# Performance work log

Hardware: AMD Instinct MI355X
Metric: run time of the kernel (lower is better)

The kernel has to match this reference:

```python
import jax, jax.numpy as jnp
import numpy as np

DIM = 256      # C
TOPK = 32      # topk_win_num
WIN = 8        # winSize
G = 64         # g (shift group size); 4*G == DIM here


def setup_inputs() -> dict:
    key = jax.random.key(0)
    k0, k1, k2, k3 = jax.random.split(key, 4)
    B, Nt, Ns, C = 32, 256, 4096, DIM
    z = jax.random.normal(k0, (B, Nt, C), jnp.float32)
    x = jax.random.normal(k1, (B, Ns, C), jnp.float32)
    # shift_op_down: Conv2d(C, 4g, 1) -> weight [4g, C]; shift_op_up: Conv2d(4g, C, 1)
    Wd = jax.random.normal(k2, (4 * G, C), jnp.float32) * 0.05
    bd = jnp.zeros((4 * G,), jnp.float32)
    Wu = jax.random.normal(k3, (C, 4 * G), jnp.float32) * 0.05
    bu = jnp.zeros((C,), jnp.float32)
    return {"z": z, "x": x, "Wd": Wd, "bd": bd, "Wu": Wu, "bu": bu}


def reference(z, x, Wd, bd, Wu, bu):
    B, Nt, C = z.shape
    Ns = x.shape[1]
    hs = int(np.sqrt(Ns))
    wn = hs // WIN          # windows per side
    wsa = WIN * WIN         # tokens per window
    K = TOPK

    # AdaptiveMaxPool2d((1,1)) over template tokens -> global max per channel
    z_max = jnp.max(z, axis=1)                               # [B, C]
    sim = jnp.einsum('bc,bnc->bn', z_max, x) / C             # [B, Ns]
    # per-window mean similarity
    sim = sim.reshape(B, wn, WIN, wn, WIN).transpose(0, 1, 3, 2, 4)
    sim = sim.reshape(B, wn * wn, wsa).mean(-1)              # [B, wn*wn]
    idx = jax.lax.top_k(sim, K)[1]                           # [B, K]

    # windowed view of search tokens: [B, wn*wn, wsa, C]
    x_win = x.reshape(B, wn, WIN, wn, WIN, C).transpose(0, 1, 3, 2, 4, 5)
    x_win = x_win.reshape(B, wn * wn, wsa, C)
    x_sel = jnp.take_along_axis(x_win, idx[:, :, None, None], axis=1)  # [B, K, wsa, C]

    xe = x_sel.reshape(B * K, WIN, WIN, C)                   # NHWC per selected window
    t = xe @ Wd.T + bd                                       # 1x1 conv down -> [n, h, w, 4G]

    # 4-direction spatial shift by 1 (zero fill), one channel group per direction
    g0, g1, g2, g3 = t[..., :G], t[..., G:2 * G], t[..., 2 * G:3 * G], t[..., 3 * G:]
    s0 = jnp.pad(g0[:, :, 1:, :], ((0, 0), (0, 0), (0, 1), (0, 0)))  # shift left  (W)
    s1 = jnp.pad(g1[:, :, :-1, :], ((0, 0), (0, 0), (1, 0), (0, 0)))  # shift right (W)
    s2 = jnp.pad(g2[:, 1:, :, :], ((0, 0), (0, 1), (0, 0), (0, 0)))  # shift up    (H)
    s3 = jnp.pad(g3[:, :-1, :, :], ((0, 0), (1, 0), (0, 0), (0, 0)))  # shift down  (H)
    sh = jnp.concatenate([s0, s1, s2, s3], axis=-1)          # [n, h, w, 4G]

    up = sh @ Wu.T + bu                                      # 1x1 conv up -> [n, h, w, C]
    out = (xe + up).reshape(B, K * WIN * WIN, C)             # [B, K*wsa, C]
    return out
```

## Files before the change

### kernel.cpp

```cpp
#include <hip/hip_runtime.h>
#include <hip/hip_bf16.h>

#define C_DIM 256
#define B_SZ 32
#define NS 4096
#define NT_Z 256
#define TOPK_K 32
#define NWIN 64
#define WTOK 64

typedef __attribute__((ext_vector_type(8))) short short8;
typedef __attribute__((ext_vector_type(4))) float f32x4;

static __device__ inline unsigned short f2b(float f) {
  union { float f; unsigned int u; } x; x.f = f;
  unsigned int u = x.u;
  return (unsigned short)((u + 0x7FFFu + ((u >> 16) & 1u)) >> 16);
}
static __device__ inline float b2f(unsigned int h16) {
  union { unsigned int u; float f; } x; x.u = h16 << 16;
  return x.f;
}

__global__ void prep_kernel(const float* __restrict__ Wd, const float* __restrict__ Wu,
                            unsigned short* __restrict__ Wdb, unsigned short* __restrict__ Wub,
                            const float* __restrict__ z, float* __restrict__ zpart) {
  int blk = blockIdx.x;
  if (blk < 64) {
    int i = blk * 256 + threadIdx.x;
    float4 a = ((const float4*)Wd)[i];
    float4 c = ((const float4*)Wu)[i];
    ushort4 ha, hc;
    ha.x = f2b(a.x); ha.y = f2b(a.y); ha.z = f2b(a.z); ha.w = f2b(a.w);
    hc.x = f2b(c.x); hc.y = f2b(c.y); hc.z = f2b(c.z); hc.w = f2b(c.w);
    ((ushort4*)Wdb)[i] = ha;
    ((ushort4*)Wub)[i] = hc;
  } else {
    int i = blk - 64;
    int b = i >> 3, ch = i & 7;
    int c = threadIdx.x;
    const float* p = z + ((size_t)b * NT_Z + ch * 32) * C_DIM + c;
    float m = p[0];
    for (int n = 1; n < 32; ++n) m = fmaxf(m, p[(size_t)n * C_DIM]);
    zpart[(size_t)i * C_DIM + c] = m;
  }
}

__global__ __launch_bounds__(256) void winscore_kernel(const float* __restrict__ x,
                                                       const float* __restrict__ zpart,
                                                       float* __restrict__ score) {
  int b = blockIdx.x >> 6;
  int w = blockIdx.x & 63;
  int wy = w >> 3, wx = w & 7;

  __shared__ float zs[C_DIM];
  {
    float m = zpart[(size_t)(b * 8) * C_DIM + threadIdx.x];
    #pragma unroll
    for (int ch = 1; ch < 8; ++ch)
      m = fmaxf(m, zpart[(size_t)(b * 8 + ch) * C_DIM + threadIdx.x]);
    zs[threadIdx.x] = m;
  }
  __syncthreads();

  int wv = threadIdx.x >> 6;
  int ln = threadIdx.x & 63;

  float a0 = 0.f, a1 = 0.f, a2 = 0.f, a3 = 0.f;
  for (int t = 0; t < 16; ++t) {
    int tok = wv * 16 + t;
    int iy = tok >> 3, ix = tok & 7;
    int n = (wy * 8 + iy) * 64 + wx * 8 + ix;
    const float4 v = *(const float4*)(x + ((size_t)b * NS + n) * C_DIM + ln * 4);
    a0 += v.x; a1 += v.y; a2 += v.z; a3 += v.w;
  }
  const float4 z4 = ((const float4*)zs)[ln];
  float p = a0 * z4.x + a1 * z4.y + a2 * z4.z + a3 * z4.w;
  for (int off = 32; off >= 1; off >>= 1) p += __shfl_xor(p, off);

  __shared__ float wsum[4];
  if (ln == 0) wsum[wv] = p;
  __syncthreads();
  if (threadIdx.x == 0) score[blockIdx.x] = wsum[0] + wsum[1] + wsum[2] + wsum[3];
}

__global__ __launch_bounds__(256, 3) void fused_win(
    const float* __restrict__ x, const float* __restrict__ score,
    const unsigned short* __restrict__ Wdb, const unsigned short* __restrict__ Wub,
    const float* __restrict__ bd, const float* __restrict__ bu,
    float* __restrict__ out)
{
  __shared__ unsigned short buf[WTOK * C_DIM];
  __shared__ float sc[NWIN];
  __shared__ int wsel_s;

  const int bk = blockIdx.x;
  const int b = bk >> 5;
  const int kk = bk & 31;
  const int tid = threadIdx.x;

  if (tid < NWIN) sc[tid] = score[b * NWIN + tid];
  __syncthreads();
  if (tid < NWIN) {
    float v = sc[tid];
    int rank = 0;
    #pragma unroll
    for (int j = 0; j < NWIN; ++j) {
      float sj = sc[j];
      rank += (sj > v) || (sj == v && j < tid);
    }
    if (rank == kk) wsel_s = tid;
  }
  __syncthreads();
  const int wsel = wsel_s;
  const int wy = wsel >> 3, wx = wsel & 7;

  {
    const int c4 = tid & 63;
    const int m0 = tid >> 6;
    const float* xb = x + (size_t)b * NS * C_DIM + c4 * 4;
    #pragma unroll 4
    for (int i = 0; i < 16; ++i) {
      int m = m0 + i * 4;
      int n = (wy * 8 + (m >> 3)) * 64 + wx * 8 + (m & 7);
      const float4 v = *(const float4*)(xb + (size_t)n * C_DIM);
      ushort4 h;
      h.x = f2b(v.x); h.y = f2b(v.y); h.z = f2b(v.z); h.w = f2b(v.w);
      int byteoff = m * 512 + ((c4 * 8) ^ ((m & 7) << 4));
      *(ushort4*)((char*)buf + byteoff) = h;
    }
  }
  __syncthreads();

  const int wv = tid >> 6;
  const int ln = tid & 63;
  const int lr = ln & 15;
  const int lg = ln >> 4;

  const unsigned short* wdbase = Wdb + ((wv * 4) * 16 + lr) * C_DIM + lg * 8;
  const unsigned short* wubase = Wub + ((wv * 4) * 16 + lr) * C_DIM + lg * 8;

  f32x4 acc[4][4];
  #pragma unroll
  for (int a = 0; a < 4; ++a)
    #pragma unroll
    for (int n2 = 0; n2 < 4; ++n2) acc[a][n2] = (f32x4){0.f, 0.f, 0.f, 0.f};

  #pragma unroll 2
  for (int ks = 0; ks < 8; ++ks) {
    short8 bf[4];
    #pragma unroll
    for (int nt = 0; nt < 4; ++nt)
      bf[nt] = *(const short8*)(wdbase + nt * 16 * C_DIM + ks * 32);
    const int kb = ks * 64 + lg * 16;
    short8 af[4];
    #pragma unroll
    for (int mt = 0; mt < 4; ++mt) {
      int m = mt * 16 + lr;
      af[mt] = *(const short8*)((const char*)buf + m * 512 + (kb ^ ((m & 7) << 4)));
    }
    #pragma unroll
    for (int mt = 0; mt < 4; ++mt)
      #pragma unroll
      for (int nt = 0; nt < 4; ++nt)
        acc[mt][nt] = __builtin_amdgcn_mfma_f32_16x16x32_bf16(af[mt], bf[nt], acc[mt][nt], 0, 0, 0);
  }

  unsigned int res[4][4][2];
  #pragma unroll
  for (int mt = 0; mt < 4; ++mt) {
    #pragma unroll
    for (int nt = 0; nt < 4; ++nt) {
      int c = wv * 64 + nt * 16 + lr;
      #pragma unroll
      for (int j = 0; j < 2; ++j) {
        int m0 = mt * 16 + lg * 4 + 2 * j;
        unsigned int lo = *(const unsigned short*)((const char*)buf + m0 * 512 + ((c * 2) ^ ((m0 & 7) << 4)));
        unsigned int hi = *(const unsigned short*)((const char*)buf + (m0 + 1) * 512 + ((c * 2) ^ (((m0 + 1) & 7) << 4)));
        res[mt][nt][j] = lo | (hi << 16);
      }
    }
  }
  __syncthreads();

  #pragma unroll
  for (int nt = 0; nt < 4; ++nt) {
    int o = wv * 64 + nt * 16 + lr;
    float bdv = bd[o];
    #pragma unroll
    for (int mt = 0; mt < 4; ++mt) {
      #pragma unroll
      for (int r = 0; r < 4; ++r) {
        int m = mt * 16 + lg * 4 + r;
        float v = acc[mt][nt][r] + bdv;
        *(unsigned short*)((char*)buf + m * 512 + ((o * 2) ^ ((m & 7) << 4))) = f2b(v);
      }
    }
  }
  __syncthreads();

  f32x4 acc2[4][4];
  {
    float buv[4];
    #pragma unroll
    for (int nt = 0; nt < 4; ++nt) buv[nt] = bu[wv * 64 + nt * 16 + lr];
    #pragma unroll
    for (int mt = 0; mt < 4; ++mt) {
      #pragma unroll
      for (int nt = 0; nt < 4; ++nt) {
        acc2[mt][nt][0] = b2f(res[mt][nt][0] & 0xffffu) + buv[nt];
        acc2[mt][nt][1] = b2f(res[mt][nt][0] >> 16)     + buv[nt];
        acc2[mt][nt][2] = b2f(res[mt][nt][1] & 0xffffu) + buv[nt];
        acc2[mt][nt][3] = b2f(res[mt][nt][1] >> 16)     + buv[nt];
      }
    }
  }

  #pragma unroll 2
  for (int ks = 0; ks < 8; ++ks) {
    short8 bf[4];
    #pragma unroll
    for (int nt = 0; nt < 4; ++nt)
      bf[nt] = *(const short8*)(wubase + nt * 16 * C_DIM + ks * 32);
    const int g = ks >> 1;
    const int dd = ((g & 1) ? -1 : 1) * ((g & 2) ? 8 : 1);
    const int kb = ks * 64 + lg * 16;
    short8 af[4];
    #pragma unroll
    for (int mt = 0; mt < 4; ++mt) {
      int m = mt * 16 + lr;
      int pos = (g & 2) ? (m >> 3) : (m & 7);
      bool ok = (g & 1) ? (pos > 0) : (pos < 7);
      int ms = m + dd;
      ms = ms < 0 ? 0 : (ms > 63 ? 63 : ms);
      short8 v = *(const short8*)((const char*)buf + ms * 512 + (kb ^ ((ms & 7) << 4)));
      const short8 zed = {0, 0, 0, 0, 0, 0, 0, 0};
      af[mt] = ok ? v : zed;
    }
    #pragma unroll
    for (int mt = 0; mt < 4; ++mt)
      #pragma unroll
      for (int nt = 0; nt < 4; ++nt)
        acc2[mt][nt] = __builtin_amdgcn_mfma_f32_16x16x32_bf16(af[mt], bf[nt], acc2[mt][nt], 0, 0, 0);
  }

  const size_t obase = (size_t)bk * WTOK * C_DIM;
  #pragma unroll
  for (int nt = 0; nt < 4; ++nt) {
    int c = wv * 64 + nt * 16 + lr;
    #pragma unroll
    for (int mt = 0; mt < 4; ++mt) {
      #pragma unroll
      for (int r = 0; r < 4; ++r) {
        int m = mt * 16 + lg * 4 + r;
        out[obase + (size_t)m * C_DIM + c] = acc2[mt][nt][r];
      }
    }
  }
}

extern "C" void kernel_launch(void* const* d_in, const int* in_sizes, int n_in,
                              void* d_out, int out_size, void* d_ws, size_t ws_size,
                              hipStream_t stream) {
  const float* z  = (const float*)d_in[0];
  const float* x  = (const float*)d_in[1];
  const float* Wd = (const float*)d_in[2];
  const float* bd = (const float*)d_in[3];
  const float* Wu = (const float*)d_in[4];
  const float* bu = (const float*)d_in[5];
  float* out = (float*)d_out;

  char* ws = (char*)d_ws;
  unsigned short* Wdb = (unsigned short*)(ws);
  unsigned short* Wub = (unsigned short*)(ws + 131072);
  float* zpart = (float*)(ws + 262144);
  float* score = (float*)(ws + 524288);

  hipLaunchKernelGGL(prep_kernel, dim3(320), dim3(256), 0, stream, Wd, Wu, Wdb, Wub, z, zpart);
  hipLaunchKernelGGL(winscore_kernel, dim3(B_SZ * NWIN), dim3(256), 0, stream, x, zpart, score);
  hipLaunchKernelGGL(fused_win, dim3(B_SZ * TOPK_K), dim3(256), 0, stream,
                     x, score, Wdb, Wub, bd, bu, out);
}
```

Before: 95.34 us.

## Preload weight fragments into registers and split LDS into separate input and intermediate buffers

Loads all down-projection weight fragments into registers before the x gather, and prefetches the up-projection weights before the barrier. Uses separate LDS buffers for the bf16 input window and the intermediate, so the residual is read from LDS at output time instead of being packed into registers early. The x gather now issues all 16 loads before converting them. The aim is to overlap global latency with other work and remove a barrier, at the cost of doubled LDS use, many more live registers, and occupancy lowered from 3 to 2 blocks.

```diff
diff --git a/kernel.cpp b/kernel.cpp
--- a/kernel.cpp
+++ b/kernel.cpp
@@ -84,13 +84,14 @@
   if (threadIdx.x == 0) score[blockIdx.x] = wsum[0] + wsum[1] + wsum[2] + wsum[3];
 }
 
-__global__ __launch_bounds__(256, 3) void fused_win(
+__global__ __launch_bounds__(256, 2) void fused_win(
     const float* __restrict__ x, const float* __restrict__ score,
     const unsigned short* __restrict__ Wdb, const unsigned short* __restrict__ Wub,
     const float* __restrict__ bd, const float* __restrict__ bu,
     float* __restrict__ out)
 {
-  __shared__ unsigned short buf[WTOK * C_DIM];
+  __shared__ unsigned short xe_s[WTOK * C_DIM];
+  __shared__ unsigned short t_s[WTOK * C_DIM];
   __shared__ float sc[NWIN];
   __shared__ int wsel_s;
 
@@ -115,30 +116,42 @@
   const int wsel = wsel_s;
   const int wy = wsel >> 3, wx = wsel & 7;
 
+  const int wv = tid >> 6;
+  const int ln = tid & 63;
+  const int lr = ln & 15;
+  const int lg = ln >> 4;
+
+  const unsigned short* wdbase = Wdb + ((wv * 4) * 16 + lr) * C_DIM + lg * 8;
+  const unsigned short* wubase = Wub + ((wv * 4) * 16 + lr) * C_DIM + lg * 8;
+
+  short8 wreg[8][4];
+  #pragma unroll
+  for (int ks = 0; ks < 8; ++ks)
+    #pragma unroll
+    for (int nt = 0; nt < 4; ++nt)
+      wreg[ks][nt] = *(const short8*)(wdbase + nt * 16 * C_DIM + ks * 32);
+
   {
     const int c4 = tid & 63;
     const int m0 = tid >> 6;
     const float* xb = x + (size_t)b * NS * C_DIM + c4 * 4;
-    #pragma unroll 4
+    float4 xv[16];
+    #pragma unroll
     for (int i = 0; i < 16; ++i) {
       int m = m0 + i * 4;
       int n = (wy * 8 + (m >> 3)) * 64 + wx * 8 + (m & 7);
-      const float4 v = *(const float4*)(xb + (size_t)n * C_DIM);
+      xv[i] = *(const float4*)(xb + (size_t)n * C_DIM);
+    }
+    #pragma unroll
+    for (int i = 0; i < 16; ++i) {
+      int m = m0 + i * 4;
       ushort4 h;
-      h.x = f2b(v.x); h.y = f2b(v.y); h.z = f2b(v.z); h.w = f2b(v.w);
+      h.x = f2b(xv[i].x); h.y = f2b(xv[i].y); h.z = f2b(xv[i].z); h.w = f2b(xv[i].w);
       int byteoff = m * 512 + ((c4 * 8) ^ ((m & 7) << 4));
-      *(ushort4*)((char*)buf + byteoff) = h;
-    }
-  }
-  __syncthreads();
-
-  const int wv = tid >> 6;
-  const int ln = tid & 63;
-  const int lr = ln & 15;
-  const int lg = ln >> 4;
-
-  const unsigned short* wdbase = Wdb + ((wv * 4) * 16 + lr) * C_DIM + lg * 8;
-  const unsigned short* wubase = Wub + ((wv * 4) * 16 + lr) * C_DIM + lg * 8;
+      *(ushort4*)((char*)xe_s + byteoff) = h;
+    }
+  }
+  __syncthreads();
 
   f32x4 acc[4][4];
   #pragma unroll
@@ -146,42 +159,21 @@
     #pragma unroll
     for (int n2 = 0; n2 < 4; ++n2) acc[a][n2] = (f32x4){0.f, 0.f, 0.f, 0.f};
 
-  #pragma unroll 2
+  #pragma unroll
   for (int ks = 0; ks < 8; ++ks) {
-    short8 bf[4];
-    #pragma unroll
-    for (int nt = 0; nt < 4; ++nt)
-      bf[nt] = *(const short8*)(wdbase + nt * 16 * C_DIM + ks * 32);
     const int kb = ks * 64 + lg * 16;
     short8 af[4];
     #pragma unroll
     for (int mt = 0; mt < 4; ++mt) {
       int m = mt * 16 + lr;
-      af[mt] = *(const short8*)((const char*)buf + m * 512 + (kb ^ ((m & 7) << 4)));
+      af[mt] = *(const short8*)((const char*)xe_s + m * 512 + (kb ^ ((m & 7) << 4)));
     }
     #pragma unroll
     for (int mt = 0; mt < 4; ++mt)
       #pragma unroll
       for (int nt = 0; nt < 4; ++nt)
-        acc[mt][nt] = __builtin_amdgcn_mfma_f32_16x16x32_bf16(af[mt], bf[nt], acc[mt][nt], 0, 0, 0);
-  }
-
-  unsigned int res[4][4][2];
-  #pragma unroll
-  for (int mt = 0; mt < 4; ++mt) {
-    #pragma unroll
-    for (int nt = 0; nt < 4; ++nt) {
-      int c = wv * 64 + nt * 16 + lr;
-      #pragma unroll
-      for (int j = 0; j < 2; ++j) {
-        int m0 = mt * 16 + lg * 4 + 2 * j;
-        unsigned int lo = *(const unsigned short*)((const char*)buf + m0 * 512 + ((c * 2) ^ ((m0 & 7) << 4)));
-        unsigned int hi = *(const unsigned short*)((const char*)buf + (m0 + 1) * 512 + ((c * 2) ^ (((m0 + 1) & 7) << 4)));
-        res[mt][nt][j] = lo | (hi << 16);
-      }
-    }
-  }
-  __syncthreads();
+        acc[mt][nt] = __builtin_amdgcn_mfma_f32_16x16x32_bf16(af[mt], wreg[ks][nt], acc[mt][nt], 0, 0, 0);
+  }
 
   #pragma unroll
   for (int nt = 0; nt < 4; ++nt) {
@@ -193,35 +185,28 @@
       for (int r = 0; r < 4; ++r) {
         int m = mt * 16 + lg * 4 + r;
         float v = acc[mt][nt][r] + bdv;
-        *(unsigned short*)((char*)buf + m * 512 + ((o * 2) ^ ((m & 7) << 4))) = f2b(v);
+        *(unsigned short*)((char*)t_s + m * 512 + ((o * 2) ^ ((m & 7) << 4))) = f2b(v);
       }
     }
   }
+
+  short8 wreg2[8][4];
+  #pragma unroll
+  for (int ks = 0; ks < 8; ++ks)
+    #pragma unroll
+    for (int nt = 0; nt < 4; ++nt)
+      wreg2[ks][nt] = *(const short8*)(wubase + nt * 16 * C_DIM + ks * 32);
+
   __syncthreads();
 
   f32x4 acc2[4][4];
-  {
-    float buv[4];
-    #pragma unroll
-    for (int nt = 0; nt < 4; ++nt) buv[nt] = bu[wv * 64 + nt * 16 + lr];
-    #pragma unroll
-    for (int mt = 0; mt < 4; ++mt) {
-      #pragma unroll
-      for (int nt = 0; nt < 4; ++nt) {
-        acc2[mt][nt][0] = b2f(res[mt][nt][0] & 0xffffu) + buv[nt];
-        acc2[mt][nt][1] = b2f(res[mt][nt][0] >> 16)     + buv[nt];
-        acc2[mt][nt][2] = b2f(res[mt][nt][1] & 0xffffu) + buv[nt];
-        acc2[mt][nt][3] = b2f(res[mt][nt][1] >> 16)     + buv[nt];
-      }
-    }
-  }
-
-  #pragma unroll 2
+  #pragma unroll
+  for (int a = 0; a < 4; ++a)
+    #pragma unroll
+    for (int n2 = 0; n2 < 4; ++n2) acc2[a][n2] = (f32x4){0.f, 0.f, 0.f, 0.f};
+
+  #pragma unroll
   for (int ks = 0; ks < 8; ++ks) {
-    short8 bf[4];
-    #pragma unroll
-    for (int nt = 0; nt < 4; ++nt)
-      bf[nt] = *(const short8*)(wubase + nt * 16 * C_DIM + ks * 32);
     const int g = ks >> 1;
     const int dd = ((g & 1) ? -1 : 1) * ((g & 2) ? 8 : 1);
     const int kb = ks * 64 + lg * 16;
@@ -233,7 +218,7 @@
       bool ok = (g & 1) ? (pos > 0) : (pos < 7);
       int ms = m + dd;
       ms = ms < 0 ? 0 : (ms > 63 ? 63 : ms);
-      short8 v = *(const short8*)((const char*)buf + ms * 512 + (kb ^ ((ms & 7) << 4)));
+      short8 v = *(const short8*)((const char*)t_s + ms * 512 + (kb ^ ((ms & 7) << 4)));
       const short8 zed = {0, 0, 0, 0, 0, 0, 0, 0};
       af[mt] = ok ? v : zed;
     }
@@ -241,19 +226,22 @@
     for (int mt = 0; mt < 4; ++mt)
       #pragma unroll
       for (int nt = 0; nt < 4; ++nt)
-        acc2[mt][nt] = __builtin_amdgcn_mfma_f32_16x16x32_bf16(af[mt], bf[nt], acc2[mt][nt], 0, 0, 0);
+        acc2[mt][nt] = __builtin_amdgcn_mfma_f32_16x16x32_bf16(af[mt], wreg2[ks][nt], acc2[mt][nt], 0, 0, 0);
   }
 
   const size_t obase = (size_t)bk * WTOK * C_DIM;
   #pragma unroll
   for (int nt = 0; nt < 4; ++nt) {
     int c = wv * 64 + nt * 16 + lr;
+    float buv = bu[c];
     #pragma unroll
     for (int mt = 0; mt < 4; ++mt) {
       #pragma unroll
       for (int r = 0; r < 4; ++r) {
         int m = mt * 16 + lg * 4 + r;
-        out[obase + (size_t)m * C_DIM + c] = acc2[mt][nt][r];
+        unsigned int xb =
+            *(const unsigned short*)((const char*)xe_s + m * 512 + ((c * 2) ^ ((m & 7) << 4)));
+        out[obase + (size_t)m * C_DIM + c] = b2f(xb) + acc2[mt][nt][r] + buv;
       }
     }
   }
```

New measurement: 82.46 us. 1.16x faster.

## Prefetch weights in register ring, batch x loads, stage output through LDS

Applied to the files above, without the earlier changes.

Weight fragments for both GEMMs are now kept in a three-slot register ring that is loaded ahead of use, and MFMA blocks are wrapped in s_setprio raises. The x gather issues eight float4 loads before converting any of them, which raises memory-level parallelism. The output is no longer written as scattered scalar stores: it is staged in LDS as bf16 and then written back as coalesced float4 rows. This costs more registers, and rounding the final output to bf16 loses precision.

```diff
diff --git a/kernel.cpp b/kernel.cpp
--- a/kernel.cpp
+++ b/kernel.cpp
@@ -115,30 +115,52 @@
   const int wsel = wsel_s;
   const int wy = wsel >> 3, wx = wsel & 7;
 
-  {
-    const int c4 = tid & 63;
-    const int m0 = tid >> 6;
-    const float* xb = x + (size_t)b * NS * C_DIM + c4 * 4;
-    #pragma unroll 4
-    for (int i = 0; i < 16; ++i) {
-      int m = m0 + i * 4;
-      int n = (wy * 8 + (m >> 3)) * 64 + wx * 8 + (m & 7);
-      const float4 v = *(const float4*)(xb + (size_t)n * C_DIM);
-      ushort4 h;
-      h.x = f2b(v.x); h.y = f2b(v.y); h.z = f2b(v.z); h.w = f2b(v.w);
-      int byteoff = m * 512 + ((c4 * 8) ^ ((m & 7) << 4));
-      *(ushort4*)((char*)buf + byteoff) = h;
-    }
-  }
-  __syncthreads();
-
   const int wv = tid >> 6;
   const int ln = tid & 63;
   const int lr = ln & 15;
   const int lg = ln >> 4;
-
-  const unsigned short* wdbase = Wdb + ((wv * 4) * 16 + lr) * C_DIM + lg * 8;
-  const unsigned short* wubase = Wub + ((wv * 4) * 16 + lr) * C_DIM + lg * 8;
+  const int c4 = tid & 63;
+  const int m0w = tid >> 6;
+
+  const unsigned short* wdbase = Wdb + (size_t)(wv * 64 + lr) * C_DIM + lg * 8;
+  const unsigned short* wubase = Wub + (size_t)(wv * 64 + lr) * C_DIM + lg * 8;
+
+  short8 wq[3][4];
+  #pragma unroll
+  for (int p = 0; p < 3; ++p)
+    #pragma unroll
+    for (int nt = 0; nt < 4; ++nt)
+      wq[p][nt] = *(const short8*)(wdbase + nt * 16 * C_DIM + p * 32);
+
+  float bdv[4], buv[4];
+  #pragma unroll
+  for (int nt = 0; nt < 4; ++nt) {
+    bdv[nt] = bd[wv * 64 + nt * 16 + lr];
+    buv[nt] = bu[wv * 64 + nt * 16 + lr];
+  }
+
+  {
+    const float* xb = x + (size_t)b * NS * C_DIM + c4 * 4;
+    #pragma unroll
+    for (int h = 0; h < 2; ++h) {
+      float4 xv[8];
+      #pragma unroll
+      for (int i = 0; i < 8; ++i) {
+        int m = m0w + (h * 8 + i) * 4;
+        int n = (wy * 8 + (m >> 3)) * 64 + wx * 8 + (m & 7);
+        xv[i] = *(const float4*)(xb + (size_t)n * C_DIM);
+      }
+      #pragma unroll
+      for (int i = 0; i < 8; ++i) {
+        int m = m0w + (h * 8 + i) * 4;
+        ushort4 hs;
+        hs.x = f2b(xv[i].x); hs.y = f2b(xv[i].y); hs.z = f2b(xv[i].z); hs.w = f2b(xv[i].w);
+        int byteoff = m * 512 + ((c4 * 8) ^ ((m & 7) << 4));
+        *(ushort4*)((char*)buf + byteoff) = hs;
+      }
+    }
+  }
+  __syncthreads();
 
   f32x4 acc[4][4];
   #pragma unroll
@@ -146,12 +168,9 @@
     #pragma unroll
     for (int n2 = 0; n2 < 4; ++n2) acc[a][n2] = (f32x4){0.f, 0.f, 0.f, 0.f};
 
-  #pragma unroll 2
+  #pragma unroll
   for (int ks = 0; ks < 8; ++ks) {
-    short8 bf[4];
-    #pragma unroll
-    for (int nt = 0; nt < 4; ++nt)
-      bf[nt] = *(const short8*)(wdbase + nt * 16 * C_DIM + ks * 32);
+    const int slot = ks % 3;
     const int kb = ks * 64 + lg * 16;
     short8 af[4];
     #pragma unroll
@@ -159,11 +178,18 @@
       int m = mt * 16 + lr;
       af[mt] = *(const short8*)((const char*)buf + m * 512 + (kb ^ ((m & 7) << 4)));
     }
+    __builtin_amdgcn_s_setprio(1);
     #pragma unroll
     for (int mt = 0; mt < 4; ++mt)
       #pragma unroll
       for (int nt = 0; nt < 4; ++nt)
-        acc[mt][nt] = __builtin_amdgcn_mfma_f32_16x16x32_bf16(af[mt], bf[nt], acc[mt][nt], 0, 0, 0);
+        acc[mt][nt] = __builtin_amdgcn_mfma_f32_16x16x32_bf16(af[mt], wq[slot][nt], acc[mt][nt], 0, 0, 0);
+    __builtin_amdgcn_s_setprio(0);
+    if (ks + 3 < 8) {
+      #pragma unroll
+      for (int nt = 0; nt < 4; ++nt)
+        wq[slot][nt] = *(const short8*)(wdbase + nt * 16 * C_DIM + (ks + 3) * 32);
+    }
   }
 
   unsigned int res[4][4][2];
@@ -181,47 +207,45 @@
       }
     }
   }
+
+  short8 wq2[3][4];
+  #pragma unroll
+  for (int p = 0; p < 3; ++p)
+    #pragma unroll
+    for (int nt = 0; nt < 4; ++nt)
+      wq2[p][nt] = *(const short8*)(wubase + nt * 16 * C_DIM + p * 32);
+
   __syncthreads();
 
   #pragma unroll
   for (int nt = 0; nt < 4; ++nt) {
     int o = wv * 64 + nt * 16 + lr;
-    float bdv = bd[o];
     #pragma unroll
     for (int mt = 0; mt < 4; ++mt) {
       #pragma unroll
       for (int r = 0; r < 4; ++r) {
         int m = mt * 16 + lg * 4 + r;
-        float v = acc[mt][nt][r] + bdv;
-        *(unsigned short*)((char*)buf + m * 512 + ((o * 2) ^ ((m & 7) << 4))) = f2b(v);
+        *(unsigned short*)((char*)buf + m * 512 + ((o * 2) ^ ((m & 7) << 4))) = f2b(acc[mt][nt][r] + bdv[nt]);
       }
     }
   }
   __syncthreads();
 
   f32x4 acc2[4][4];
-  {
-    float buv[4];
-    #pragma unroll
-    for (int nt = 0; nt < 4; ++nt) buv[nt] = bu[wv * 64 + nt * 16 + lr];
-    #pragma unroll
-    for (int mt = 0; mt < 4; ++mt) {
-      #pragma unroll
-      for (int nt = 0; nt < 4; ++nt) {
-        acc2[mt][nt][0] = b2f(res[mt][nt][0] & 0xffffu) + buv[nt];
-        acc2[mt][nt][1] = b2f(res[mt][nt][0] >> 16)     + buv[nt];
-        acc2[mt][nt][2] = b2f(res[mt][nt][1] & 0xffffu) + buv[nt];
-        acc2[mt][nt][3] = b2f(res[mt][nt][1] >> 16)     + buv[nt];
-      }
-    }
-  }
-
-  #pragma unroll 2
+  #pragma unroll
+  for (int mt = 0; mt < 4; ++mt) {
+    #pragma unroll
+    for (int nt = 0; nt < 4; ++nt) {
+      acc2[mt][nt][0] = b2f(res[mt][nt][0] & 0xffffu) + buv[nt];
+      acc2[mt][nt][1] = b2f(res[mt][nt][0] >> 16)     + buv[nt];
+      acc2[mt][nt][2] = b2f(res[mt][nt][1] & 0xffffu) + buv[nt];
+      acc2[mt][nt][3] = b2f(res[mt][nt][1] >> 16)     + buv[nt];
+    }
+  }
+
+  #pragma unroll
   for (int ks = 0; ks < 8; ++ks) {
-    short8 bf[4];
-    #pragma unroll
-    for (int nt = 0; nt < 4; ++nt)
-      bf[nt] = *(const short8*)(wubase + nt * 16 * C_DIM + ks * 32);
+    const int slot = ks % 3;
     const int g = ks >> 1;
     const int dd = ((g & 1) ? -1 : 1) * ((g & 2) ? 8 : 1);
     const int kb = ks * 64 + lg * 16;
@@ -237,14 +261,21 @@
       const short8 zed = {0, 0, 0, 0, 0, 0, 0, 0};
       af[mt] = ok ? v : zed;
     }
+    __builtin_amdgcn_s_setprio(1);
     #pragma unroll
     for (int mt = 0; mt < 4; ++mt)
       #pragma unroll
       for (int nt = 0; nt < 4; ++nt)
-        acc2[mt][nt] = __builtin_amdgcn_mfma_f32_16x16x32_bf16(af[mt], bf[nt], acc2[mt][nt], 0, 0, 0);
-  }
-
-  const size_t obase = (size_t)bk * WTOK * C_DIM;
+        acc2[mt][nt] = __builtin_amdgcn_mfma_f32_16x16x32_bf16(af[mt], wq2[slot][nt], acc2[mt][nt], 0, 0, 0);
+    __builtin_amdgcn_s_setprio(0);
+    if (ks + 3 < 8) {
+      #pragma unroll
+      for (int nt = 0; nt < 4; ++nt)
+        wq2[slot][nt] = *(const short8*)(wubase + nt * 16 * C_DIM + (ks + 3) * 32);
+    }
+  }
+  __syncthreads();
+
   #pragma unroll
   for (int nt = 0; nt < 4; ++nt) {
     int c = wv * 64 + nt * 16 + lr;
@@ -253,8 +284,22 @@
       #pragma unroll
       for (int r = 0; r < 4; ++r) {
         int m = mt * 16 + lg * 4 + r;
-        out[obase + (size_t)m * C_DIM + c] = acc2[mt][nt][r];
-      }
+        *(unsigned short*)((char*)buf + m * 512 + ((c * 2) ^ ((m & 7) << 4))) = f2b(acc2[mt][nt][r]);
+      }
+    }
+  }
+  __syncthreads();
+
+  {
+    float* ob = out + (size_t)bk * WTOK * C_DIM + c4 * 4;
+    #pragma unroll
+    for (int i = 0; i < 16; ++i) {
+      int m = m0w + i * 4;
+      int off = m * 512 + ((c4 * 8) ^ ((m & 7) << 4));
+      ushort4 s4 = *(const ushort4*)((const char*)buf + off);
+      float4 o;
+      o.x = b2f(s4.x); o.y = b2f(s4.y); o.z = b2f(s4.z); o.w = b2f(s4.w);
+      *(float4*)(ob + (size_t)m * C_DIM) = o;
     }
   }
 }
```

After: 170.5 us. 1.79x slower.
